# Kernel tuning notes

Hardware: AMD Instinct MI355X
Metric: run time of the kernel (lower is better)

Reference implementation:

```python
import jax, jax.numpy as jnp
import numpy as np

COMMITMENT_COST = 0.25
EPS = 1e-10


def setup_inputs() -> dict:
    key = jax.random.key(0)
    k1, k2 = jax.random.split(key)
    x = jax.random.normal(k1, (64, 4096, 64), dtype=jnp.float32)          # [B, T, D]
    embedding = jax.random.normal(k2, (512, 64), dtype=jnp.float32)       # [K, D] codebook
    return {"x": x, "embedding": embedding}


def reference(x, embedding):
    B, T, D = x.shape
    K = embedding.shape[0]
    flat = x.reshape(-1, D)                                               # [N, D]
    N = flat.shape[0]

    distances = (jnp.sum(flat * flat, axis=1, keepdims=True)
                 - 2.0 * (flat @ embedding.T)
                 + jnp.sum(embedding * embedding, axis=1))

    idx = jnp.argmin(distances, axis=1)                                   # [N] nearest code
    quantized = embedding[idx].reshape(x.shape)                           # gather lookup

    # commitment loss (EMA variant: only e_latent_loss, codebook frozen w.r.t. loss)
    e_latent_loss = jnp.mean((jax.lax.stop_gradient(quantized) - x) ** 2)
    loss = COMMITMENT_COST * e_latent_loss

    # straight-through estimator
    q_st = x + jax.lax.stop_gradient(quantized - x)

    # perplexity via scatter-add histogram of code usage
    counts = jnp.zeros((K,), dtype=x.dtype).at[idx].add(jnp.ones((), x.dtype))
    avg_probs = counts / jnp.asarray(N, x.dtype)
    perplexity = jnp.exp(-jnp.sum(avg_probs * jnp.log(avg_probs + EPS)))

    return q_st, loss, perplexity
```

## Files before the change

### kernel.cpp

```cpp
#include <hip/hip_runtime.h>
#include <math.h>

#define N_ROWS   262144
#define DIM      64
#define KCODES   512
#define MT       64
#define NTHREADS 256
#define NBLOCKS  (N_ROWS / MT)
#define XS_STRIDE 68
#define ES_STRIDE 72
#define MARGIN   2e-3f

typedef float f32x4 __attribute__((ext_vector_type(4)));
typedef short s16x8 __attribute__((ext_vector_type(8)));


__device__ __forceinline__ unsigned short f2bf(float f) {
    unsigned u = __float_as_uint(f);
    unsigned r = u + 0x7fffu + ((u >> 16) & 1u);
    return (unsigned short)(r >> 16);
}
__device__ __forceinline__ float bf2f(unsigned short h) {
    return __uint_as_float(((unsigned)h) << 16);
}

__global__ __launch_bounds__(512) void vq_prep(const float* __restrict__ emb,
                                               float* __restrict__ esq,
                                               int* __restrict__ counts,
                                               float* __restrict__ lossAdj,
                                               unsigned short* __restrict__ eh,
                                               unsigned short* __restrict__ el,
                                               unsigned* __restrict__ mask) {
    int k = threadIdx.x;
    const float* e = emb + (size_t)k * DIM;
    float s = 0.f;
    #pragma unroll
    for (int d = 0; d < DIM; ++d) s += e[d] * e[d];
    esq[k] = s;
    counts[k] = 0;
    #pragma unroll
    for (int d = 0; d < DIM; ++d) {
        float v = e[d];
        unsigned short h = f2bf(v);
        eh[k * DIM + d] = h;
        el[k * DIM + d] = f2bf(v - bf2f(h));
    }
    #pragma unroll
    for (int i = 0; i < 16; ++i) mask[k * 16 + i] = 0u;
    if (k == 0) *lossAdj = 0.f;
}

__global__ __launch_bounds__(NTHREADS, 2) void vq_main(
    const float* __restrict__ x, const float* __restrict__ emb,
    const float* __restrict__ g_esq,
    const unsigned short* __restrict__ eh_g, const unsigned short* __restrict__ el_g,
    unsigned short* __restrict__ g_idx, float* __restrict__ g_lossPart,
    unsigned* __restrict__ g_mask, float* __restrict__ out)
{
    __shared__ float xs[MT * XS_STRIDE];
    __shared__ unsigned short ehs[128 * ES_STRIDE];
    __shared__ unsigned short els[128 * ES_STRIDE];
    __shared__ float esq_s[KCODES];
    __shared__ int   idx_s[MT];
    __shared__ int   flg_s[MT];
    __shared__ float wred[4];

    const int tid  = threadIdx.x;
    const int R0   = blockIdx.x * MT;
    const int w    = tid >> 6;
    const int lane = tid & 63;
    const int m    = lane & 15;
    const int q    = lane >> 4;

    #pragma unroll
    for (int i = 0; i < 4; ++i) {
        int flat = tid + NTHREADS * i;
        int r  = flat >> 4;
        int qc = flat & 15;
        f32x4 v = *(const f32x4*)&x[(size_t)(R0 + r) * DIM + 4 * qc];
        *(f32x4*)&xs[r * XS_STRIDE + 4 * qc] = v;
    }
    esq_s[tid]       = g_esq[tid];
    esq_s[tid + 256] = g_esq[tid + 256];
    __syncthreads();

    s16x8 axh[2], axl[2];
    const int lrow = w * 16 + m;
    #pragma unroll
    for (int kc = 0; kc < 2; ++kc) {
        const float* px = &xs[lrow * XS_STRIDE + kc * 32 + q * 8];
        s16x8 h, l;
        #pragma unroll
        for (int t = 0; t < 8; ++t) {
            float v = px[t];
            unsigned short hb = f2bf(v);
            h[t] = (short)hb;
            l[t] = (short)f2bf(v - bf2f(hb));
        }
        axh[kc] = h; axl[kc] = l;
    }

    f32x4 acc[32];
    #pragma unroll
    for (int a = 0; a < 32; ++a) acc[a] = (f32x4){0.f, 0.f, 0.f, 0.f};

    for (int c = 0; c < 4; ++c) {
        if (c) __syncthreads();
        #pragma unroll
        for (int i = 0; i < 4; ++i) {
            int ch = tid + NTHREADS * i;
            int rl = ch >> 3, off = (ch & 7) * 8;
            size_t gofs = (size_t)(c * 128 + rl) * DIM + off;
            *(s16x8*)&ehs[rl * ES_STRIDE + off] = *(const s16x8*)&eh_g[gofs];
            *(s16x8*)&els[rl * ES_STRIDE + off] = *(const s16x8*)&el_g[gofs];
        }
        __syncthreads();
        #pragma unroll
        for (int ct = 0; ct < 8; ++ct) {
            const int a = c * 8 + ct;
            #pragma unroll
            for (int kc = 0; kc < 2; ++kc) {
                const int bofs = (ct * 16 + m) * ES_STRIDE + kc * 32 + q * 8;
                s16x8 bh = *(const s16x8*)&ehs[bofs];
                s16x8 bl = *(const s16x8*)&els[bofs];
                acc[a] = __builtin_amdgcn_mfma_f32_16x16x32_bf16(axh[kc], bh, acc[a], 0, 0, 0);
                acc[a] = __builtin_amdgcn_mfma_f32_16x16x32_bf16(axl[kc], bh, acc[a], 0, 0, 0);
                acc[a] = __builtin_amdgcn_mfma_f32_16x16x32_bf16(axh[kc], bl, acc[a], 0, 0, 0);
            }
        }
    }

    float b1[4], b2[4]; int i1[4];
    #pragma unroll
    for (int r = 0; r < 4; ++r) { b1[r] = 3.4e38f; b2[r] = 3.4e38f; i1[r] = 0; }
    #pragma unroll
    for (int a = 0; a < 32; ++a) {
        int col = a * 16 + m;
        float e2 = esq_s[col];
        #pragma unroll
        for (int r = 0; r < 4; ++r) {
            float dist = e2 - 2.f * acc[a][r];
            if (dist < b1[r]) { b2[r] = b1[r]; b1[r] = dist; i1[r] = col; }
            else if (dist < b2[r]) b2[r] = dist;
        }
    }
    #pragma unroll
    for (int s = 1; s < 16; s <<= 1) {
        #pragma unroll
        for (int r = 0; r < 4; ++r) {
            float ob1 = __shfl_xor(b1[r], s);
            int   oi1 = __shfl_xor(i1[r], s);
            float ob2 = __shfl_xor(b2[r], s);
            bool owin = (ob1 < b1[r]) || (ob1 == b1[r] && oi1 < i1[r]);
            float lb1 = owin ? b1[r] : ob1;
            b2[r] = fminf(fminf(b2[r], ob2), lb1);
            if (owin) { b1[r] = ob1; i1[r] = oi1; }
        }
    }
    if (m == 0) {
        #pragma unroll
        for (int r = 0; r < 4; ++r) {
            int lrw = w * 16 + q * 4 + r;
            idx_s[lrw] = i1[r];
            int f = (b2[r] - b1[r] < MARGIN) ? 1 : 0;
            flg_s[lrw] = f;
            if (f) {
                int grow = R0 + lrw;
                atomicOr(&g_mask[grow >> 5], 1u << (grow & 31));
            }
        }
    }
    __syncthreads();
    if (tid < MT) g_idx[R0 + tid] = (unsigned short)idx_s[tid];

    const int r  = tid >> 2;
    const int d0 = (tid & 3) * 16;
    float lpart = 0.f;
    if (!flg_s[r]) {
        const int ki = idx_s[r];
        const float* erow = emb + (size_t)ki * DIM;
        #pragma unroll
        for (int s4 = 0; s4 < 4; ++s4) {
            int d = d0 + 4 * s4;
            f32x4 e4 = *(const f32x4*)&erow[d];
            float xv0 = xs[r * XS_STRIDE + d + 0];
            float xv1 = xs[r * XS_STRIDE + d + 1];
            float xv2 = xs[r * XS_STRIDE + d + 2];
            float xv3 = xs[r * XS_STRIDE + d + 3];
            float f0 = e4.x - xv0, f1 = e4.y - xv1, f2 = e4.z - xv2, f3 = e4.w - xv3;
            f32x4 o = {xv0 + f0, xv1 + f1, xv2 + f2, xv3 + f3};
            *(f32x4*)&out[(size_t)(R0 + r) * DIM + d] = o;
            lpart += f0*f0 + f1*f1 + f2*f2 + f3*f3;
        }
    }
    #pragma unroll
    for (int off = 32; off > 0; off >>= 1) lpart += __shfl_down(lpart, off);
    if ((tid & 63) == 0) wred[tid >> 6] = lpart;
    __syncthreads();
    if (tid == 0) g_lossPart[blockIdx.x] = wred[0] + wred[1] + wred[2] + wred[3];
}

__global__ __launch_bounds__(256) void vq_cleanup(
    const float* __restrict__ x, const float* __restrict__ emb,
    const float* __restrict__ g_esq, unsigned short* __restrict__ g_idx,
    float* __restrict__ lossAdj, const unsigned* __restrict__ g_mask,
    float* __restrict__ out)
{
    int w    = blockIdx.x * 4 + (threadIdx.x >> 6);
    int lane = threadIdx.x & 63;
    unsigned m0 = g_mask[w * 2], m1 = g_mask[w * 2 + 1];
    unsigned long long bits = ((unsigned long long)m1 << 32) | m0;
    while (bits) {
        int b = __ffsll((unsigned long long)bits) - 1;
        bits &= bits - 1;
        int row = w * 64 + b;
        const float* xr = &x[(size_t)row * DIM];
        float best = 3.4e38f; int bidx = 0;
        #pragma unroll
        for (int j = 0; j < 8; ++j) {
            int c = lane * 8 + j;
            const float* er = &emb[(size_t)c * DIM];
            float dot = 0.f;
            #pragma unroll
            for (int d = 0; d < DIM; ++d) dot = fmaf(xr[d], er[d], dot);
            float dist = g_esq[c] - 2.f * dot;
            if (dist < best) { best = dist; bidx = c; }
        }
        #pragma unroll
        for (int s = 1; s < 64; s <<= 1) {
            float ob = __shfl_xor(best, s);
            int   oi = __shfl_xor(bidx, s);
            if (ob < best || (ob == best && oi < bidx)) { best = ob; bidx = oi; }
        }
        float xv = xr[lane];
        float ev = emb[(size_t)bidx * DIM + lane];
        float f  = ev - xv;
        out[(size_t)row * DIM + lane] = xv + f;
        float lp = f * f;
        #pragma unroll
        for (int s = 1; s < 64; s <<= 1) lp += __shfl_xor(lp, s);
        if (lane == 0) {
            atomicAdd(lossAdj, lp);
            g_idx[row] = (unsigned short)bidx;
        }
    }
}

__global__ __launch_bounds__(256) void vq_hist(const unsigned short* __restrict__ g_idx,
                                               int* __restrict__ counts) {
    __shared__ int h[KCODES];
    int t = threadIdx.x;
    h[t] = 0; h[t + 256] = 0;
    __syncthreads();
    const unsigned short* p = g_idx + (size_t)blockIdx.x * 4096;
    #pragma unroll
    for (int i = 0; i < 16; ++i)
        atomicAdd(&h[p[t + 256 * i]], 1);
    __syncthreads();
    int v0 = h[t], v1 = h[t + 256];
    if (v0) atomicAdd(&counts[t], v0);
    if (v1) atomicAdd(&counts[t + 256], v1);
}

__global__ __launch_bounds__(512) void vq_final(const int* __restrict__ counts,
                                                const float* __restrict__ lossPart,
                                                const float* __restrict__ lossAdj,
                                                float* __restrict__ out) {
    __shared__ float redp[8];
    __shared__ float redl[8];
    int k = threadIdx.x;
    float p = (float)counts[k] * (1.f / 262144.f);
    float t = p * logf(p + 1e-10f);
    float l = 0.f;
    #pragma unroll
    for (int i = 0; i < 8; ++i) l += lossPart[k + 512 * i];
    #pragma unroll
    for (int off = 32; off > 0; off >>= 1) {
        t += __shfl_down(t, off);
        l += __shfl_down(l, off);
    }
    if ((k & 63) == 0) { redp[k >> 6] = t; redl[k >> 6] = l; }
    __syncthreads();
    if (k == 0) {
        float s = 0.f, ls = 0.f;
        #pragma unroll
        for (int i = 0; i < 8; ++i) { s += redp[i]; ls += redl[i]; }
        out[16777216] = (ls + *lossAdj) * (0.25f / 16777216.f);
        out[16777217] = expf(-s);
    }
}

extern "C" void kernel_launch(void* const* d_in, const int* in_sizes, int n_in,
                              void* d_out, int out_size, void* d_ws, size_t ws_size,
                              hipStream_t stream) {
    const float* x   = (const float*)d_in[0];
    const float* emb = (const float*)d_in[1];
    float* out = (float*)d_out;

    char* ws = (char*)d_ws;
    float*          esq      = (float*)(ws + 0);
    int*            counts   = (int*)(ws + 2048);
    float*          lossAdj  = (float*)(ws + 4096);
    unsigned short* eh       = (unsigned short*)(ws + 4608);
    unsigned short* el       = (unsigned short*)(ws + 70144);
    unsigned*       mask     = (unsigned*)(ws + 135680);
    unsigned short* gidx     = (unsigned short*)(ws + 168448);
    float*          lossPart = (float*)(ws + 692736);

    vq_prep<<<1, 512, 0, stream>>>(emb, esq, counts, lossAdj, eh, el, mask);
    vq_main<<<NBLOCKS, NTHREADS, 0, stream>>>(x, emb, esq, eh, el,
                                              gidx, lossPart, mask, out);
    vq_cleanup<<<1024, 256, 0, stream>>>(x, emb, esq, gidx, lossAdj, mask, out);
    vq_hist<<<64, 256, 0, stream>>>(gidx, counts);
    vq_final<<<1, 512, 0, stream>>>(counts, lossPart, lossAdj, out);
}
```

Baseline: 264.3 us.

## Make vq_main persistent with whole codebook resident in LDS

```diff
diff --git a/kernel.cpp b/kernel.cpp
--- a/kernel.cpp
+++ b/kernel.cpp
@@ -4,15 +4,17 @@
 #define N_ROWS   262144
 #define DIM      64
 #define KCODES   512
-#define MT       64
 #define NTHREADS 256
-#define NBLOCKS  (N_ROWS / MT)
-#define XS_STRIDE 68
-#define ES_STRIDE 72
+#define NBLOCKS  256
+#define ROWS_PER_BLOCK (N_ROWS / NBLOCKS)
+#define ROWS_PER_WAVE  (ROWS_PER_BLOCK / 4)
+#define TILES_PER_WAVE (ROWS_PER_WAVE / 32)
+#define ESTR     72
 #define MARGIN   2e-3f
 
 typedef float f32x4 __attribute__((ext_vector_type(4)));
 typedef short s16x8 __attribute__((ext_vector_type(8)));
+typedef short s16x4 __attribute__((ext_vector_type(4)));
 
 
 __device__ __forceinline__ unsigned short f2bf(float f) {
@@ -28,8 +30,6 @@
                                                float* __restrict__ esq,
                                                int* __restrict__ counts,
                                                float* __restrict__ lossAdj,
-                                               unsigned short* __restrict__ eh,
-                                               unsigned short* __restrict__ el,
                                                unsigned* __restrict__ mask) {
     int k = threadIdx.x;
     const float* e = emb + (size_t)k * DIM;
@@ -39,165 +39,173 @@
     esq[k] = s;
     counts[k] = 0;
     #pragma unroll
-    for (int d = 0; d < DIM; ++d) {
-        float v = e[d];
-        unsigned short h = f2bf(v);
-        eh[k * DIM + d] = h;
-        el[k * DIM + d] = f2bf(v - bf2f(h));
-    }
-    #pragma unroll
     for (int i = 0; i < 16; ++i) mask[k * 16 + i] = 0u;
     if (k == 0) *lossAdj = 0.f;
 }
 
-__global__ __launch_bounds__(NTHREADS, 2) void vq_main(
+__global__ __launch_bounds__(NTHREADS, 1) void vq_main(
     const float* __restrict__ x, const float* __restrict__ emb,
     const float* __restrict__ g_esq,
-    const unsigned short* __restrict__ eh_g, const unsigned short* __restrict__ el_g,
     unsigned short* __restrict__ g_idx, float* __restrict__ g_lossPart,
     unsigned* __restrict__ g_mask, float* __restrict__ out)
 {
-    __shared__ float xs[MT * XS_STRIDE];
-    __shared__ unsigned short ehs[128 * ES_STRIDE];
-    __shared__ unsigned short els[128 * ES_STRIDE];
+    __shared__ unsigned short ehs[KCODES * ESTR];
+    __shared__ unsigned short els[KCODES * ESTR];
     __shared__ float esq_s[KCODES];
-    __shared__ int   idx_s[MT];
-    __shared__ int   flg_s[MT];
-    __shared__ float wred[4];
+    __shared__ int idxflg[4 * 32];
 
     const int tid  = threadIdx.x;
-    const int R0   = blockIdx.x * MT;
     const int w    = tid >> 6;
     const int lane = tid & 63;
     const int m    = lane & 15;
     const int q    = lane >> 4;
 
-    #pragma unroll
-    for (int i = 0; i < 4; ++i) {
-        int flat = tid + NTHREADS * i;
-        int r  = flat >> 4;
-        int qc = flat & 15;
-        f32x4 v = *(const f32x4*)&x[(size_t)(R0 + r) * DIM + 4 * qc];
-        *(f32x4*)&xs[r * XS_STRIDE + 4 * qc] = v;
+    #pragma unroll 4
+    for (int i = 0; i < 32; ++i) {
+        int f = tid + NTHREADS * i;
+        int code = f >> 4, d4 = (f & 15) * 4;
+        f32x4 v = *(const f32x4*)&emb[(size_t)code * DIM + d4];
+        s16x4 hv, lv;
+        #pragma unroll
+        for (int j = 0; j < 4; ++j) {
+            unsigned short h = f2bf(v[j]);
+            hv[j] = (short)h;
+            lv[j] = (short)f2bf(v[j] - bf2f(h));
+        }
+        *(s16x4*)&ehs[code * ESTR + d4] = hv;
+        *(s16x4*)&els[code * ESTR + d4] = lv;
     }
     esq_s[tid]       = g_esq[tid];
     esq_s[tid + 256] = g_esq[tid + 256];
     __syncthreads();
 
-    s16x8 axh[2], axl[2];
-    const int lrow = w * 16 + m;
-    #pragma unroll
-    for (int kc = 0; kc < 2; ++kc) {
-        const float* px = &xs[lrow * XS_STRIDE + kc * 32 + q * 8];
-        s16x8 h, l;
-        #pragma unroll
-        for (int t = 0; t < 8; ++t) {
-            float v = px[t];
-            unsigned short hb = f2bf(v);
-            h[t] = (short)hb;
-            l[t] = (short)f2bf(v - bf2f(hb));
-        }
-        axh[kc] = h; axl[kc] = l;
-    }
-
-    f32x4 acc[32];
-    #pragma unroll
-    for (int a = 0; a < 32; ++a) acc[a] = (f32x4){0.f, 0.f, 0.f, 0.f};
-
-    for (int c = 0; c < 4; ++c) {
-        if (c) __syncthreads();
-        #pragma unroll
-        for (int i = 0; i < 4; ++i) {
-            int ch = tid + NTHREADS * i;
-            int rl = ch >> 3, off = (ch & 7) * 8;
-            size_t gofs = (size_t)(c * 128 + rl) * DIM + off;
-            *(s16x8*)&ehs[rl * ES_STRIDE + off] = *(const s16x8*)&eh_g[gofs];
-            *(s16x8*)&els[rl * ES_STRIDE + off] = *(const s16x8*)&el_g[gofs];
-        }
-        __syncthreads();
-        #pragma unroll
-        for (int ct = 0; ct < 8; ++ct) {
-            const int a = c * 8 + ct;
+    float lpart = 0.f;
+    const int waveRow0 = blockIdx.x * ROWS_PER_BLOCK + w * ROWS_PER_WAVE;
+
+    for (int t = 0; t < TILES_PER_WAVE; ++t) {
+        const int T0 = waveRow0 + t * 32;
+
+        s16x8 axh[2][2], axl[2][2];
+        #pragma unroll
+        for (int g = 0; g < 2; ++g) {
+            const float* px = &x[(size_t)(T0 + g * 16 + m) * DIM + q * 8];
             #pragma unroll
             for (int kc = 0; kc < 2; ++kc) {
-                const int bofs = (ct * 16 + m) * ES_STRIDE + kc * 32 + q * 8;
-                s16x8 bh = *(const s16x8*)&ehs[bofs];
-                s16x8 bl = *(const s16x8*)&els[bofs];
-                acc[a] = __builtin_amdgcn_mfma_f32_16x16x32_bf16(axh[kc], bh, acc[a], 0, 0, 0);
-                acc[a] = __builtin_amdgcn_mfma_f32_16x16x32_bf16(axl[kc], bh, acc[a], 0, 0, 0);
-                acc[a] = __builtin_amdgcn_mfma_f32_16x16x32_bf16(axh[kc], bl, acc[a], 0, 0, 0);
-            }
-        }
-    }
-
-    float b1[4], b2[4]; int i1[4];
-    #pragma unroll
-    for (int r = 0; r < 4; ++r) { b1[r] = 3.4e38f; b2[r] = 3.4e38f; i1[r] = 0; }
-    #pragma unroll
-    for (int a = 0; a < 32; ++a) {
-        int col = a * 16 + m;
-        float e2 = esq_s[col];
-        #pragma unroll
-        for (int r = 0; r < 4; ++r) {
-            float dist = e2 - 2.f * acc[a][r];
-            if (dist < b1[r]) { b2[r] = b1[r]; b1[r] = dist; i1[r] = col; }
-            else if (dist < b2[r]) b2[r] = dist;
-        }
-    }
-    #pragma unroll
-    for (int s = 1; s < 16; s <<= 1) {
-        #pragma unroll
-        for (int r = 0; r < 4; ++r) {
-            float ob1 = __shfl_xor(b1[r], s);
-            int   oi1 = __shfl_xor(i1[r], s);
-            float ob2 = __shfl_xor(b2[r], s);
-            bool owin = (ob1 < b1[r]) || (ob1 == b1[r] && oi1 < i1[r]);
-            float lb1 = owin ? b1[r] : ob1;
-            b2[r] = fminf(fminf(b2[r], ob2), lb1);
-            if (owin) { b1[r] = ob1; i1[r] = oi1; }
-        }
-    }
-    if (m == 0) {
-        #pragma unroll
-        for (int r = 0; r < 4; ++r) {
-            int lrw = w * 16 + q * 4 + r;
-            idx_s[lrw] = i1[r];
-            int f = (b2[r] - b1[r] < MARGIN) ? 1 : 0;
-            flg_s[lrw] = f;
-            if (f) {
-                int grow = R0 + lrw;
-                atomicOr(&g_mask[grow >> 5], 1u << (grow & 31));
-            }
-        }
-    }
-    __syncthreads();
-    if (tid < MT) g_idx[R0 + tid] = (unsigned short)idx_s[tid];
-
-    const int r  = tid >> 2;
-    const int d0 = (tid & 3) * 16;
-    float lpart = 0.f;
-    if (!flg_s[r]) {
-        const int ki = idx_s[r];
-        const float* erow = emb + (size_t)ki * DIM;
-        #pragma unroll
-        for (int s4 = 0; s4 < 4; ++s4) {
-            int d = d0 + 4 * s4;
-            f32x4 e4 = *(const f32x4*)&erow[d];
-            float xv0 = xs[r * XS_STRIDE + d + 0];
-            float xv1 = xs[r * XS_STRIDE + d + 1];
-            float xv2 = xs[r * XS_STRIDE + d + 2];
-            float xv3 = xs[r * XS_STRIDE + d + 3];
-            float f0 = e4.x - xv0, f1 = e4.y - xv1, f2 = e4.z - xv2, f3 = e4.w - xv3;
-            f32x4 o = {xv0 + f0, xv1 + f1, xv2 + f2, xv3 + f3};
-            *(f32x4*)&out[(size_t)(R0 + r) * DIM + d] = o;
-            lpart += f0*f0 + f1*f1 + f2*f2 + f3*f3;
-        }
-    }
-    #pragma unroll
-    for (int off = 32; off > 0; off >>= 1) lpart += __shfl_down(lpart, off);
-    if ((tid & 63) == 0) wred[tid >> 6] = lpart;
-    __syncthreads();
-    if (tid == 0) g_lossPart[blockIdx.x] = wred[0] + wred[1] + wred[2] + wred[3];
+                f32x4 v0 = *(const f32x4*)&px[kc * 32];
+                f32x4 v1 = *(const f32x4*)&px[kc * 32 + 4];
+                s16x8 h, l;
+                #pragma unroll
+                for (int j = 0; j < 4; ++j) {
+                    unsigned short hb = f2bf(v0[j]);
+                    h[j] = (short)hb; l[j] = (short)f2bf(v0[j] - bf2f(hb));
+                    unsigned short hb1 = f2bf(v1[j]);
+                    h[4 + j] = (short)hb1; l[4 + j] = (short)f2bf(v1[j] - bf2f(hb1));
+                }
+                axh[g][kc] = h; axl[g][kc] = l;
+            }
+        }
+
+        f32x4 acc0[32], acc1[32];
+        #pragma unroll
+        for (int a = 0; a < 32; ++a) { acc0[a] = (f32x4){0,0,0,0}; acc1[a] = (f32x4){0,0,0,0}; }
+
+        #pragma unroll
+        for (int ct = 0; ct < 32; ++ct) {
+            const int bo = (ct * 16 + m) * ESTR + q * 8;
+            s16x8 bh0 = *(const s16x8*)&ehs[bo];
+            s16x8 bl0 = *(const s16x8*)&els[bo];
+            s16x8 bh1 = *(const s16x8*)&ehs[bo + 32];
+            s16x8 bl1 = *(const s16x8*)&els[bo + 32];
+            acc0[ct] = __builtin_amdgcn_mfma_f32_16x16x32_bf16(axh[0][0], bh0, acc0[ct], 0, 0, 0);
+            acc0[ct] = __builtin_amdgcn_mfma_f32_16x16x32_bf16(axl[0][0], bh0, acc0[ct], 0, 0, 0);
+            acc0[ct] = __builtin_amdgcn_mfma_f32_16x16x32_bf16(axh[0][0], bl0, acc0[ct], 0, 0, 0);
+            acc0[ct] = __builtin_amdgcn_mfma_f32_16x16x32_bf16(axh[0][1], bh1, acc0[ct], 0, 0, 0);
+            acc0[ct] = __builtin_amdgcn_mfma_f32_16x16x32_bf16(axl[0][1], bh1, acc0[ct], 0, 0, 0);
+            acc0[ct] = __builtin_amdgcn_mfma_f32_16x16x32_bf16(axh[0][1], bl1, acc0[ct], 0, 0, 0);
+            acc1[ct] = __builtin_amdgcn_mfma_f32_16x16x32_bf16(axh[1][0], bh0, acc1[ct], 0, 0, 0);
+            acc1[ct] = __builtin_amdgcn_mfma_f32_16x16x32_bf16(axl[1][0], bh0, acc1[ct], 0, 0, 0);
+            acc1[ct] = __builtin_amdgcn_mfma_f32_16x16x32_bf16(axh[1][0], bl0, acc1[ct], 0, 0, 0);
+            acc1[ct] = __builtin_amdgcn_mfma_f32_16x16x32_bf16(axh[1][1], bh1, acc1[ct], 0, 0, 0);
+            acc1[ct] = __builtin_amdgcn_mfma_f32_16x16x32_bf16(axl[1][1], bh1, acc1[ct], 0, 0, 0);
+            acc1[ct] = __builtin_amdgcn_mfma_f32_16x16x32_bf16(axh[1][1], bl1, acc1[ct], 0, 0, 0);
+        }
+
+        #pragma unroll
+        for (int g = 0; g < 2; ++g) {
+            float b1[4], b2[4]; int i1[4];
+            #pragma unroll
+            for (int r = 0; r < 4; ++r) { b1[r] = 3.4e38f; b2[r] = 3.4e38f; i1[r] = 0; }
+            #pragma unroll
+            for (int a = 0; a < 32; ++a) {
+                int col = a * 16 + m;
+                float e2 = esq_s[col];
+                #pragma unroll
+                for (int r = 0; r < 4; ++r) {
+                    f32x4 av = (g == 0) ? acc0[a] : acc1[a];
+                    float dist = e2 - 2.f * av[r];
+                    if (dist < b1[r]) { b2[r] = b1[r]; b1[r] = dist; i1[r] = col; }
+                    else if (dist < b2[r]) b2[r] = dist;
+                }
+            }
+            #pragma unroll
+            for (int s = 1; s < 16; s <<= 1) {
+                #pragma unroll
+                for (int r = 0; r < 4; ++r) {
+                    float ob1 = __shfl_xor(b1[r], s);
+                    int   oi1 = __shfl_xor(i1[r], s);
+                    float ob2 = __shfl_xor(b2[r], s);
+                    bool owin = (ob1 < b1[r]) || (ob1 == b1[r] && oi1 < i1[r]);
+                    float lb1 = owin ? b1[r] : ob1;
+                    b2[r] = fminf(fminf(b2[r], ob2), lb1);
+                    if (owin) { b1[r] = ob1; i1[r] = oi1; }
+                }
+            }
+            if (m == 0) {
+                #pragma unroll
+                for (int r = 0; r < 4; ++r) {
+                    int fl = (b2[r] - b1[r] < MARGIN) ? 1 : 0;
+                    idxflg[w * 32 + g * 16 + q * 4 + r] = i1[r] | (fl << 16);
+                    if (fl) {
+                        int grow = T0 + g * 16 + q * 4 + r;
+                        atomicOr(&g_mask[grow >> 5], 1u << (grow & 31));
+                    }
+                }
+            }
+        }
+        __threadfence_block();
+
+        #pragma unroll
+        for (int g = 0; g < 2; ++g) {
+            int row16 = lane >> 2;
+            int pk  = idxflg[w * 32 + g * 16 + row16];
+            int row = T0 + g * 16 + row16;
+            int ki  = pk & 0xffff;
+            int fl  = pk >> 16;
+            if ((lane & 3) == 0) g_idx[row] = (unsigned short)ki;
+            if (!fl) {
+                int c = (lane & 3) * 16;
+                const float* xr = &x[(size_t)row * DIM + c];
+                const float* er = &emb[(size_t)ki * DIM + c];
+                #pragma unroll
+                for (int u = 0; u < 4; ++u) {
+                    f32x4 xv = *(const f32x4*)&xr[4 * u];
+                    f32x4 ev = *(const f32x4*)&er[4 * u];
+                    f32x4 fd, o;
+                    #pragma unroll
+                    for (int j = 0; j < 4; ++j) {
+                        fd[j] = ev[j] - xv[j];
+                        o[j]  = xv[j] + fd[j];
+                        lpart += fd[j] * fd[j];
+                    }
+                    *(f32x4*)&out[(size_t)row * DIM + c + 4 * u] = o;
+                }
+            }
+        }
+    }
+
+    #pragma unroll
+    for (int s = 32; s > 0; s >>= 1) lpart += __shfl_down(lpart, s);
+    if (lane == 0) g_lossPart[blockIdx.x * 4 + w] = lpart;
 }
 
 __global__ __launch_bounds__(256) void vq_cleanup(
@@ -271,9 +279,7 @@
     int k = threadIdx.x;
     float p = (float)counts[k] * (1.f / 262144.f);
     float t = p * logf(p + 1e-10f);
-    float l = 0.f;
-    #pragma unroll
-    for (int i = 0; i < 8; ++i) l += lossPart[k + 512 * i];
+    float l = lossPart[k] + lossPart[k + 512];
     #pragma unroll
     for (int off = 32; off > 0; off >>= 1) {
         t += __shfl_down(t, off);
@@ -301,15 +307,12 @@
     float*          esq      = (float*)(ws + 0);
     int*            counts   = (int*)(ws + 2048);
     float*          lossAdj  = (float*)(ws + 4096);
-    unsigned short* eh       = (unsigned short*)(ws + 4608);
-    unsigned short* el       = (unsigned short*)(ws + 70144);
-    unsigned*       mask     = (unsigned*)(ws + 135680);
-    unsigned short* gidx     = (unsigned short*)(ws + 168448);
-    float*          lossPart = (float*)(ws + 692736);
-
-    vq_prep<<<1, 512, 0, stream>>>(emb, esq, counts, lossAdj, eh, el, mask);
-    vq_main<<<NBLOCKS, NTHREADS, 0, stream>>>(x, emb, esq, eh, el,
-                                              gidx, lossPart, mask, out);
+    unsigned*       mask     = (unsigned*)(ws + 4608);
+    unsigned short* gidx     = (unsigned short*)(ws + 37376);
+    float*          lossPart = (float*)(ws + 561664);
+
+    vq_prep<<<1, 512, 0, stream>>>(emb, esq, counts, lossAdj, mask);
+    vq_main<<<NBLOCKS, NTHREADS, 0, stream>>>(x, emb, esq, gidx, lossPart, mask, out);
     vq_cleanup<<<1024, 256, 0, stream>>>(x, emb, esq, gidx, lossAdj, mask, out);
     vq_hist<<<64, 256, 0, stream>>>(gidx, counts);
     vq_final<<<1, 512, 0, stream>>>(counts, lossPart, lossAdj, out);
```

After: 346.6 us. 31.2% more time.
